# Kernel tuning notes

Hardware: AMD Instinct MI355X
Metric: run time of the kernel (lower is better)

Reference implementation:

```python
import jax, jax.numpy as jnp
import numpy as np

B, NI, NO = 4, 256, 256          # batch, num_in, num_out
DIN, DQ, DH, DOUT = 256, 256, 256, 256


def setup_inputs() -> dict:
    key = jax.random.key(0)
    ks = jax.random.split(key, 6)
    def w(k, shape, fan_in):
        return jax.random.normal(k, shape, jnp.float32) / np.sqrt(fan_in).astype(np.float32)
    return {
        "x": jax.random.normal(ks[0], (B, NI, DIN), jnp.float32),
        "query": jax.random.normal(ks[1], (B, NO, DQ), jnp.float32),
        # pre_cond_mlp: Linear(DIN -> DH)
        "W_pre": w(ks[2], (DIN, DH), DIN), "b_pre": jnp.zeros((DH,), jnp.float32),
        # cond_embed: Linear(DQ -> DH)
        "W_emb": w(ks[3], (DQ, DH), DQ), "b_emb": jnp.zeros((DH,), jnp.float32),
        # post_cond_mlp: Linear(2*DH -> DH) + GELU + Linear(DH -> DOUT)
        "W1": w(ks[4], (2 * DH, DH), 2 * DH), "b1": jnp.zeros((DH,), jnp.float32),
        "W2": w(ks[5], (DH, DOUT), DH), "b2": jnp.zeros((DOUT,), jnp.float32),
    }


def reference(x, query, W_pre, b_pre, W_emb, b_emb, W1, b1, W2, b2):
    # pre_cond_mlp(x): [B, NI, DH]
    xp = x @ W_pre + b_pre
    # cond_embed(query): [B, NO, DH]
    c = query @ W_emb + b_emb
    # Original torch code: repeat xp over NO, c over NI, concat -> [B,NI,NO,2*DH],
    # then Linear(2*DH->DH). Algebraically identical (and far cheaper) to split W1
    # and broadcast-add the two projections:
    W1x, W1c = W1[:DH], W1[DH:]          # [DH, DH] each
    h = (xp @ W1x)[:, :, None, :] + (c @ W1c)[:, None, :, :] + b1  # [B, NI, NO, DH]
    h = jax.nn.gelu(h, approximate=False)  # torch nn.GELU default = exact erf
    return h @ W2 + b2                     # [B, NI, NO, DOUT]
```

## Files before the change

kernel.cpp:

```cpp
#include <hip/hip_runtime.h>
#include <hip/hip_bf16.h>
#include <cstdint>
#include <cstddef>


typedef __bf16  bf16x8 __attribute__((ext_vector_type(8)));
typedef float   f32x16 __attribute__((ext_vector_type(16)));

__device__ __forceinline__ float fast_gelu(float x) {
    const float x2 = x * x;
    const float t  = __builtin_fmaf(x2, 0.07135481283f, 1.5957691216f);
    const float e  = __builtin_amdgcn_exp2f(x * t * -1.442695041f);
    return x * __builtin_amdgcn_rcpf(1.0f + e);
}

__global__ __launch_bounds__(256) void prep_kernel(
    const float* __restrict__ x, const float* __restrict__ query,
    const float* __restrict__ W_pre, const float* __restrict__ b_pre,
    const float* __restrict__ W_emb, const float* __restrict__ b_emb,
    const float* __restrict__ W1, const float* __restrict__ b1,
    const float* __restrict__ W2,
    float* __restrict__ u, float* __restrict__ v,
    unsigned short* __restrict__ w2t)
{
    const int b = blockIdx.x;
    const int t = threadIdx.x;

    if (b >= 512) {
        const int n0 = (b - 512) * 4;
        const float4 wv = *reinterpret_cast<const float4*>(W2 + (size_t)t * 256 + n0);
        const float vals[4] = {wv.x, wv.y, wv.z, wv.w};
#pragma unroll
        for (int j = 0; j < 4; ++j) {
            const __bf16 bv = (__bf16)vals[j];
            w2t[(size_t)(n0 + j) * 256 + t] = __builtin_bit_cast(unsigned short, bv);
        }
        return;
    }

    const bool isq = (b >= 256);
    const float* __restrict__ A   = isq ? query : x;
    const float* __restrict__ Wa  = isq ? W_emb : W_pre;
    const float* __restrict__ ba  = isq ? b_emb : b_pre;
    const float* __restrict__ W1p = isq ? (W1 + 256 * 256) : W1;
    float* __restrict__ outp      = isq ? v : u;
    const int r0 = (isq ? (b - 256) : b) * 4;

    __shared__ float as[4][256];
    __shared__ float xs[4][256];

#pragma unroll
    for (int r = 0; r < 4; ++r)
        as[r][t] = A[(size_t)(r0 + r) * 256 + t];
    __syncthreads();

    float acc[4] = {0.f, 0.f, 0.f, 0.f};
    for (int k = 0; k < 256; ++k) {
        const float wv = Wa[(size_t)k * 256 + t];
#pragma unroll
        for (int r = 0; r < 4; ++r) acc[r] += as[r][k] * wv;
    }
    const float bav = ba[t];
#pragma unroll
    for (int r = 0; r < 4; ++r) xs[r][t] = acc[r] + bav;
    __syncthreads();

    float acc2[4] = {0.f, 0.f, 0.f, 0.f};
    for (int k = 0; k < 256; ++k) {
        const float wv = W1p[(size_t)k * 256 + t];
#pragma unroll
        for (int r = 0; r < 4; ++r) acc2[r] += xs[r][k] * wv;
    }
    const float b1v = isq ? 0.f : b1[t];
#pragma unroll
    for (int r = 0; r < 4; ++r)
        outp[(size_t)(r0 + r) * 256 + t] = acc2[r] + b1v;
}

__global__ __launch_bounds__(256, 2) void fused_kernel(
    const float* __restrict__ U, const float* __restrict__ V,
    const unsigned short* __restrict__ W2T, const float* __restrict__ b2,
    float* __restrict__ out)
{
    __shared__ uint4 wlds[2048];

    const int t    = threadIdx.x;
    const int lane = t & 63;
    const int w    = t >> 6;
    const int l31  = lane & 31;
    const int hi   = lane >> 5;

    const size_t r0 = (size_t)blockIdx.x * 128;
    const int bb = (int)(r0 >> 16);
    const int ii = (int)((r0 >> 8) & 255);
    const int j0 = (int)(r0 & 255);

    const float* __restrict__ urow = U + ((size_t)(bb * 256 + ii)) * 256;
    const int jA = j0 + w * 32 + l31;
    const float* __restrict__ vrow = V + ((size_t)(bb * 256 + jA)) * 256;

    f32x16 acc[8];
#pragma unroll
    for (int i = 0; i < 8; ++i) acc[i] = (f32x16)0.f;

    for (int kk = 0; kk < 256; kk += 64) {
        __syncthreads();
#pragma unroll
        for (int it = 0; it < 8; ++it) {
            const int idx = it * 256 + t;
            const int n   = idx >> 3;
            const int g   = idx & 7;
            wlds[n * 8 + (g ^ (n & 7))] = *reinterpret_cast<const uint4*>(
                W2T + (size_t)n * 256 + kk + g * 8);
        }
        __syncthreads();

#pragma unroll
        for (int s = 0; s < 4; ++s) {
            const int k0 = kk + s * 16;
            const float4 u0 = *reinterpret_cast<const float4*>(urow + k0 + hi * 8);
            const float4 u1 = *reinterpret_cast<const float4*>(urow + k0 + hi * 8 + 4);
            const float4 v0 = *reinterpret_cast<const float4*>(vrow + k0 + hi * 8);
            const float4 v1 = *reinterpret_cast<const float4*>(vrow + k0 + hi * 8 + 4);
            const float hv[8] = {u0.x + v0.x, u0.y + v0.y, u0.z + v0.z, u0.w + v0.w,
                                 u1.x + v1.x, u1.y + v1.y, u1.z + v1.z, u1.w + v1.w};
            bf16x8 afrag;
#pragma unroll
            for (int e = 0; e < 8; ++e)
                afrag[e] = (__bf16)fast_gelu(hv[e]);

            const int gk = s * 2 + hi;
#pragma unroll
            for (int cg = 0; cg < 8; ++cg) {
                const int col = cg * 32 + l31;
                const bf16x8 bfrag = __builtin_bit_cast(
                    bf16x8, wlds[col * 8 + (gk ^ (col & 7))]);
                acc[cg] = __builtin_amdgcn_mfma_f32_32x32x16_bf16(
                    afrag, bfrag, acc[cg], 0, 0, 0);
            }
        }
    }

#pragma unroll
    for (int cg = 0; cg < 8; ++cg) {
        const int col = cg * 32 + l31;
        const float bv = b2[col];
#pragma unroll
        for (int r = 0; r < 16; ++r) {
            const int row = w * 32 + 4 * hi + (r & 3) + 8 * (r >> 2);
            out[(r0 + row) * 256 + col] = acc[cg][r] + bv;
        }
    }
}

extern "C" void kernel_launch(void* const* d_in, const int* in_sizes, int n_in,
                              void* d_out, int out_size, void* d_ws, size_t ws_size,
                              hipStream_t stream)
{
    const float* x     = (const float*)d_in[0];
    const float* query = (const float*)d_in[1];
    const float* W_pre = (const float*)d_in[2];
    const float* b_pre = (const float*)d_in[3];
    const float* W_emb = (const float*)d_in[4];
    const float* b_emb = (const float*)d_in[5];
    const float* W1    = (const float*)d_in[6];
    const float* b1    = (const float*)d_in[7];
    const float* W2    = (const float*)d_in[8];
    const float* b2    = (const float*)d_in[9];
    float* out = (float*)d_out;

    char* ws = (char*)d_ws;
    float* u            = (float*)(ws);
    float* v            = (float*)(ws + (1 << 20));
    unsigned short* w2t = (unsigned short*)(ws + 2 * (1 << 20));

    prep_kernel<<<576, 256, 0, stream>>>(x, query, W_pre, b_pre, W_emb, b_emb,
                                         W1, b1, W2, u, v, w2t);
    fused_kernel<<<2048, 256, 0, stream>>>(u, v, w2t, b2, out);
}
```

Before: 112.7 us.

## Halve fused tile rows, stage GELU activations in LDS, raise occupancy

The fused kernel now processes 64 output rows per block instead of 128. The four waves are arranged as a 2x2 grid over row and column halves, so each wave keeps 4 accumulators instead of 8. The GELU activations are computed once per element and staged in a swizzled LDS buffer, rather than recomputed per wave from global U/V. Launch bounds rise to 4 blocks per CU, GELU constants are folded to save a multiply, and output stores become nontemporal. The smaller tiles mean twice as many blocks and twice the total W2T loads into LDS.

```diff
diff --git a/kernel.cpp b/kernel.cpp
--- a/kernel.cpp
+++ b/kernel.cpp
@@ -9,8 +9,8 @@
 
 __device__ __forceinline__ float fast_gelu(float x) {
     const float x2 = x * x;
-    const float t  = __builtin_fmaf(x2, 0.07135481283f, 1.5957691216f);
-    const float e  = __builtin_amdgcn_exp2f(x * t * -1.442695041f);
+    const float m  = __builtin_fmaf(x2, -0.1029433f, -2.3022072f);
+    const float e  = __builtin_amdgcn_exp2f(x * m);
     return x * __builtin_amdgcn_rcpf(1.0f + e);
 }
 
@@ -77,34 +77,39 @@
         outp[(size_t)(r0 + r) * 256 + t] = acc2[r] + b1v;
 }
 
-__global__ __launch_bounds__(256, 2) void fused_kernel(
+__global__ __launch_bounds__(256, 4) void fused_kernel(
     const float* __restrict__ U, const float* __restrict__ V,
     const unsigned short* __restrict__ W2T, const float* __restrict__ b2,
     float* __restrict__ out)
 {
     __shared__ uint4 wlds[2048];
+    __shared__ uint4 hlds[512];
 
     const int t    = threadIdx.x;
     const int lane = t & 63;
     const int w    = t >> 6;
     const int l31  = lane & 31;
     const int hi   = lane >> 5;
+    const int rg   = w >> 1;
+    const int cgrp = w & 1;
 
-    const size_t r0 = (size_t)blockIdx.x * 128;
+    const size_t r0 = (size_t)blockIdx.x * 64;
     const int bb = (int)(r0 >> 16);
     const int ii = (int)((r0 >> 8) & 255);
     const int j0 = (int)(r0 & 255);
 
+    const int hr = t >> 2;
+    const int kq = t & 3;
     const float* __restrict__ urow = U + ((size_t)(bb * 256 + ii)) * 256;
-    const int jA = j0 + w * 32 + l31;
-    const float* __restrict__ vrow = V + ((size_t)(bb * 256 + jA)) * 256;
+    const float* __restrict__ vrow = V + ((size_t)(bb * 256 + j0 + hr)) * 256;
 
-    f32x16 acc[8];
+    const int arow = rg * 32 + l31;
+
+    f32x16 acc[4];
 #pragma unroll
-    for (int i = 0; i < 8; ++i) acc[i] = (f32x16)0.f;
+    for (int i = 0; i < 4; ++i) acc[i] = (f32x16)0.f;
 
     for (int kk = 0; kk < 256; kk += 64) {
-        __syncthreads();
 #pragma unroll
         for (int it = 0; it < 8; ++it) {
             const int idx = it * 256 + t;
@@ -113,42 +118,55 @@
             wlds[n * 8 + (g ^ (n & 7))] = *reinterpret_cast<const uint4*>(
                 W2T + (size_t)n * 256 + kk + g * 8);
         }
+        bf16x8 h0, h1;
+#pragma unroll
+        for (int m = 0; m < 4; ++m) {
+            const float4 uv = *reinterpret_cast<const float4*>(urow + kk + kq * 16 + m * 4);
+            const float4 vv = *reinterpret_cast<const float4*>(vrow + kk + kq * 16 + m * 4);
+            const float g0 = fast_gelu(uv.x + vv.x);
+            const float g1 = fast_gelu(uv.y + vv.y);
+            const float g2 = fast_gelu(uv.z + vv.z);
+            const float g3 = fast_gelu(uv.w + vv.w);
+            if (m < 2) {
+                const int e = m * 4;
+                h0[e] = (__bf16)g0; h0[e+1] = (__bf16)g1;
+                h0[e+2] = (__bf16)g2; h0[e+3] = (__bf16)g3;
+            } else {
+                const int e = (m - 2) * 4;
+                h1[e] = (__bf16)g0; h1[e+1] = (__bf16)g1;
+                h1[e+2] = (__bf16)g2; h1[e+3] = (__bf16)g3;
+            }
+        }
+        hlds[hr * 8 + ((kq * 2)     ^ (hr & 7))] = __builtin_bit_cast(uint4, h0);
+        hlds[hr * 8 + ((kq * 2 + 1) ^ (hr & 7))] = __builtin_bit_cast(uint4, h1);
         __syncthreads();
 
 #pragma unroll
         for (int s = 0; s < 4; ++s) {
-            const int k0 = kk + s * 16;
-            const float4 u0 = *reinterpret_cast<const float4*>(urow + k0 + hi * 8);
-            const float4 u1 = *reinterpret_cast<const float4*>(urow + k0 + hi * 8 + 4);
-            const float4 v0 = *reinterpret_cast<const float4*>(vrow + k0 + hi * 8);
-            const float4 v1 = *reinterpret_cast<const float4*>(vrow + k0 + hi * 8 + 4);
-            const float hv[8] = {u0.x + v0.x, u0.y + v0.y, u0.z + v0.z, u0.w + v0.w,
-                                 u1.x + v1.x, u1.y + v1.y, u1.z + v1.z, u1.w + v1.w};
-            bf16x8 afrag;
+            const int g = 2 * s + hi;
+            const bf16x8 afrag = __builtin_bit_cast(
+                bf16x8, hlds[arow * 8 + (g ^ (arow & 7))]);
 #pragma unroll
-            for (int e = 0; e < 8; ++e)
-                afrag[e] = (__bf16)fast_gelu(hv[e]);
-
-            const int gk = s * 2 + hi;
-#pragma unroll
-            for (int cg = 0; cg < 8; ++cg) {
-                const int col = cg * 32 + l31;
+            for (int cg = 0; cg < 4; ++cg) {
+                const int col = cgrp * 128 + cg * 32 + l31;
                 const bf16x8 bfrag = __builtin_bit_cast(
-                    bf16x8, wlds[col * 8 + (gk ^ (col & 7))]);
+                    bf16x8, wlds[col * 8 + (g ^ (col & 7))]);
                 acc[cg] = __builtin_amdgcn_mfma_f32_32x32x16_bf16(
                     afrag, bfrag, acc[cg], 0, 0, 0);
             }
         }
+        __syncthreads();
     }
 
 #pragma unroll
-    for (int cg = 0; cg < 8; ++cg) {
-        const int col = cg * 32 + l31;
+    for (int cg = 0; cg < 4; ++cg) {
+        const int col = cgrp * 128 + cg * 32 + l31;
         const float bv = b2[col];
 #pragma unroll
-        for (int r = 0; r < 16; ++r) {
-            const int row = w * 32 + 4 * hi + (r & 3) + 8 * (r >> 2);
-            out[(r0 + row) * 256 + col] = acc[cg][r] + bv;
+        for (int rr = 0; rr < 16; ++rr) {
+            const int row = rg * 32 + 4 * hi + (rr & 3) + 8 * (rr >> 2);
+            __builtin_nontemporal_store(acc[cg][rr] + bv,
+                                        out + (r0 + row) * 256 + col);
         }
     }
 }
@@ -176,5 +194,5 @@
 
     prep_kernel<<<576, 256, 0, stream>>>(x, query, W_pre, b_pre, W_emb, b_emb,
                                          W1, b1, W2, u, v, w2t);
-    fused_kernel<<<2048, 256, 0, stream>>>(u, v, w2t, b2, out);
+    fused_kernel<<<4096, 256, 0, stream>>>(u, v, w2t, b2, out);
 }
```

Measured after the change: 126.4 us. +12.2%, slower.

## Stage GELU activations through LDS with coalesced loads and async W2 copies

Applied to the files above, without the earlier changes.

V rows are now loaded coalesced (float2 across the 32 lanes along k) instead of each lane streaming its own row. GELU is computed once per element and packed to bf16 into a swizzled LDS tile that the MFMA A-fragments read from. W2T tiles are copied with global_load_lds direct-to-LDS transfers, the GELU constants are folded to save a multiply, and output stores become nontemporal. This adds 16KB of LDS per block, which may reduce occupancy, and moves the barriers to the end of each k-step.

```diff
diff --git a/kernel.cpp b/kernel.cpp
--- a/kernel.cpp
+++ b/kernel.cpp
@@ -9,8 +9,8 @@
 
 __device__ __forceinline__ float fast_gelu(float x) {
     const float x2 = x * x;
-    const float t  = __builtin_fmaf(x2, 0.07135481283f, 1.5957691216f);
-    const float e  = __builtin_amdgcn_exp2f(x * t * -1.442695041f);
+    const float m  = __builtin_fmaf(x2, -0.1029433f, -2.3022072f);
+    const float e  = __builtin_amdgcn_exp2f(x * m);
     return x * __builtin_amdgcn_rcpf(1.0f + e);
 }
 
@@ -83,6 +83,8 @@
     float* __restrict__ out)
 {
     __shared__ uint4 wlds[2048];
+    __shared__ uint4 hlds[1024];
+    unsigned int* const hlds32 = reinterpret_cast<unsigned int*>(hlds);
 
     const int t    = threadIdx.x;
     const int lane = t & 63;
@@ -95,41 +97,52 @@
     const int ii = (int)((r0 >> 8) & 255);
     const int j0 = (int)(r0 & 255);
 
-    const float* __restrict__ urow = U + ((size_t)(bb * 256 + ii)) * 256;
-    const int jA = j0 + w * 32 + l31;
-    const float* __restrict__ vrow = V + ((size_t)(bb * 256 + jA)) * 256;
+    const float* __restrict__ urow  = U + ((size_t)(bb * 256 + ii)) * 256;
+    const float* __restrict__ vbase = V + ((size_t)(bb * 256 + j0)) * 256;
 
     f32x16 acc[8];
 #pragma unroll
     for (int i = 0; i < 8; ++i) acc[i] = (f32x16)0.f;
 
     for (int kk = 0; kk < 256; kk += 64) {
-        __syncthreads();
 #pragma unroll
         for (int it = 0; it < 8; ++it) {
             const int idx = it * 256 + t;
             const int n   = idx >> 3;
-            const int g   = idx & 7;
-            wlds[n * 8 + (g ^ (n & 7))] = *reinterpret_cast<const uint4*>(
-                W2T + (size_t)n * 256 + kk + g * 8);
+            const int gp  = idx & 7;
+            const int g   = gp ^ (n & 7);
+            __builtin_amdgcn_global_load_lds(
+                (const __attribute__((address_space(1))) unsigned int*)
+                    (W2T + (size_t)n * 256 + kk + g * 8),
+                (__attribute__((address_space(3))) unsigned int*)
+                    (wlds + idx),
+                16, 0, 0);
+        }
+
+        const float2 uv2 = *reinterpret_cast<const float2*>(urow + kk + 2 * l31);
+        float2 vv[16];
+#pragma unroll
+        for (int p = 0; p < 16; ++p) {
+            const int row = w * 32 + p * 2 + hi;
+            vv[p] = *reinterpret_cast<const float2*>(vbase + (size_t)row * 256 + kk + 2 * l31);
+        }
+#pragma unroll
+        for (int p = 0; p < 16; ++p) {
+            const int row = w * 32 + p * 2 + hi;
+            union { unsigned int u32; __bf16 h[2]; } pk;
+            pk.h[0] = (__bf16)fast_gelu(uv2.x + vv[p].x);
+            pk.h[1] = (__bf16)fast_gelu(uv2.y + vv[p].y);
+            const int d = l31;
+            hlds32[row * 32 + (((d >> 2) ^ (row & 7)) << 2) + (d & 3)] = pk.u32;
         }
         __syncthreads();
 
 #pragma unroll
         for (int s = 0; s < 4; ++s) {
-            const int k0 = kk + s * 16;
-            const float4 u0 = *reinterpret_cast<const float4*>(urow + k0 + hi * 8);
-            const float4 u1 = *reinterpret_cast<const float4*>(urow + k0 + hi * 8 + 4);
-            const float4 v0 = *reinterpret_cast<const float4*>(vrow + k0 + hi * 8);
-            const float4 v1 = *reinterpret_cast<const float4*>(vrow + k0 + hi * 8 + 4);
-            const float hv[8] = {u0.x + v0.x, u0.y + v0.y, u0.z + v0.z, u0.w + v0.w,
-                                 u1.x + v1.x, u1.y + v1.y, u1.z + v1.z, u1.w + v1.w};
-            bf16x8 afrag;
-#pragma unroll
-            for (int e = 0; e < 8; ++e)
-                afrag[e] = (__bf16)fast_gelu(hv[e]);
-
-            const int gk = s * 2 + hi;
+            const int gk = 2 * s + hi;
+            const int arow = w * 32 + l31;
+            const bf16x8 afrag = __builtin_bit_cast(
+                bf16x8, hlds[arow * 8 + (gk ^ (arow & 7))]);
 #pragma unroll
             for (int cg = 0; cg < 8; ++cg) {
                 const int col = cg * 32 + l31;
@@ -139,6 +152,7 @@
                     afrag, bfrag, acc[cg], 0, 0, 0);
             }
         }
+        __syncthreads();
     }
 
 #pragma unroll
@@ -146,9 +160,10 @@
         const int col = cg * 32 + l31;
         const float bv = b2[col];
 #pragma unroll
-        for (int r = 0; r < 16; ++r) {
-            const int row = w * 32 + 4 * hi + (r & 3) + 8 * (r >> 2);
-            out[(r0 + row) * 256 + col] = acc[cg][r] + bv;
+        for (int rr = 0; rr < 16; ++rr) {
+            const int row = w * 32 + 4 * hi + (rr & 3) + 8 * (rr >> 2);
+            __builtin_nontemporal_store(acc[cg][rr] + bv,
+                                        out + (r0 + row) * 256 + col);
         }
     }
 }
```

Result: faster. 106.5 us (-5.5%).

## Split output columns across blocks and stage full-K W2 tile in LDS asynchronously

Applied to the files above, without the earlier changes.

Each block of the fused kernel now covers 128 rows by 128 output columns instead of 128 by 256, which doubles the grid. The block loads its whole 256-deep slice of W2 into LDS once with global_load_lds, replacing four sync-separated staging rounds with a single barrier. Output stores are marked nontemporal, and the GELU exponent constants are pre-folded to save a multiply. The trade-off is that the GELU of each U+V element is now computed in two blocks, and LDS use doubles, which may lower occupancy.

```diff
diff --git a/kernel.cpp b/kernel.cpp
--- a/kernel.cpp
+++ b/kernel.cpp
@@ -9,8 +9,8 @@
 
 __device__ __forceinline__ float fast_gelu(float x) {
     const float x2 = x * x;
-    const float t  = __builtin_fmaf(x2, 0.07135481283f, 1.5957691216f);
-    const float e  = __builtin_amdgcn_exp2f(x * t * -1.442695041f);
+    const float m  = __builtin_fmaf(x2, -0.1029433f, -2.3022072f);
+    const float e  = __builtin_amdgcn_exp2f(x * m);
     return x * __builtin_amdgcn_rcpf(1.0f + e);
 }
 
@@ -82,7 +82,7 @@
     const unsigned short* __restrict__ W2T, const float* __restrict__ b2,
     float* __restrict__ out)
 {
-    __shared__ uint4 wlds[2048];
+    __shared__ uint4 wlds[4096];
 
     const int t    = threadIdx.x;
     const int lane = t & 63;
@@ -90,65 +90,77 @@
     const int l31  = lane & 31;
     const int hi   = lane >> 5;
 
-    const size_t r0 = (size_t)blockIdx.x * 128;
-    const int bb = (int)(r0 >> 16);
-    const int ii = (int)((r0 >> 8) & 255);
-    const int j0 = (int)(r0 & 255);
-
-    const float* __restrict__ urow = U + ((size_t)(bb * 256 + ii)) * 256;
-    const int jA = j0 + w * 32 + l31;
-    const float* __restrict__ vrow = V + ((size_t)(bb * 256 + jA)) * 256;
-
-    f32x16 acc[8];
-#pragma unroll
-    for (int i = 0; i < 8; ++i) acc[i] = (f32x16)0.f;
-
-    for (int kk = 0; kk < 256; kk += 64) {
-        __syncthreads();
-#pragma unroll
-        for (int it = 0; it < 8; ++it) {
-            const int idx = it * 256 + t;
-            const int n   = idx >> 3;
-            const int g   = idx & 7;
-            wlds[n * 8 + (g ^ (n & 7))] = *reinterpret_cast<const uint4*>(
-                W2T + (size_t)n * 256 + kk + g * 8);
-        }
-        __syncthreads();
+    const int bid  = blockIdx.x;
+    const int tile = bid >> 2;
+    const int jh   = (bid >> 1) & 1;
+    const int ch   = bid & 1;
+    const int bb   = tile >> 8;
+    const int n0   = ch * 128;
+    const int j0   = jh * 128;
 
 #pragma unroll
-        for (int s = 0; s < 4; ++s) {
-            const int k0 = kk + s * 16;
-            const float4 u0 = *reinterpret_cast<const float4*>(urow + k0 + hi * 8);
-            const float4 u1 = *reinterpret_cast<const float4*>(urow + k0 + hi * 8 + 4);
-            const float4 v0 = *reinterpret_cast<const float4*>(vrow + k0 + hi * 8);
-            const float4 v1 = *reinterpret_cast<const float4*>(vrow + k0 + hi * 8 + 4);
-            const float hv[8] = {u0.x + v0.x, u0.y + v0.y, u0.z + v0.z, u0.w + v0.w,
-                                 u1.x + v1.x, u1.y + v1.y, u1.z + v1.z, u1.w + v1.w};
-            bf16x8 afrag;
+    for (int it = 0; it < 16; ++it) {
+        const int idx = it * 256 + t;
+        const int n   = idx >> 5;
+        const int gp  = idx & 31;
+        const int g   = (gp & 24) | ((gp ^ n) & 7);
+        __builtin_amdgcn_global_load_lds(
+            (const __attribute__((address_space(1))) unsigned int*)
+                (W2T + (size_t)(n0 + n) * 256 + g * 8),
+            (__attribute__((address_space(3))) unsigned int*)(wlds + idx),
+            16, 0, 0);
+    }
+
+    const float* __restrict__ urow = U + (size_t)tile * 256;
+    const float* __restrict__ vrow =
+        V + ((size_t)(bb * 256 + j0 + w * 32 + l31)) * 256;
+
+    f32x16 acc[4];
 #pragma unroll
-            for (int e = 0; e < 8; ++e)
-                afrag[e] = (__bf16)fast_gelu(hv[e]);
+    for (int i = 0; i < 4; ++i) acc[i] = (f32x16)0.f;
 
-            const int gk = s * 2 + hi;
+    __syncthreads();
+
+#pragma unroll 4
+    for (int s = 0; s < 16; ++s) {
+        const int k0 = s * 16 + hi * 8;
+        const float4 ua = *reinterpret_cast<const float4*>(urow + k0);
+        const float4 ub = *reinterpret_cast<const float4*>(urow + k0 + 4);
+        const float4 va = *reinterpret_cast<const float4*>(vrow + k0);
+        const float4 vb = *reinterpret_cast<const float4*>(vrow + k0 + 4);
+
+        bf16x8 afrag;
+        afrag[0] = (__bf16)fast_gelu(ua.x + va.x);
+        afrag[1] = (__bf16)fast_gelu(ua.y + va.y);
+        afrag[2] = (__bf16)fast_gelu(ua.z + va.z);
+        afrag[3] = (__bf16)fast_gelu(ua.w + va.w);
+        afrag[4] = (__bf16)fast_gelu(ub.x + vb.x);
+        afrag[5] = (__bf16)fast_gelu(ub.y + vb.y);
+        afrag[6] = (__bf16)fast_gelu(ub.z + vb.z);
+        afrag[7] = (__bf16)fast_gelu(ub.w + vb.w);
+
+        const int gk = 2 * s + hi;
 #pragma unroll
-            for (int cg = 0; cg < 8; ++cg) {
-                const int col = cg * 32 + l31;
-                const bf16x8 bfrag = __builtin_bit_cast(
-                    bf16x8, wlds[col * 8 + (gk ^ (col & 7))]);
-                acc[cg] = __builtin_amdgcn_mfma_f32_32x32x16_bf16(
-                    afrag, bfrag, acc[cg], 0, 0, 0);
-            }
+        for (int cg = 0; cg < 4; ++cg) {
+            const int nloc = cg * 32 + l31;
+            const int slot = (gk & 24) | ((gk ^ nloc) & 7);
+            const bf16x8 bfrag = __builtin_bit_cast(
+                bf16x8, wlds[nloc * 32 + slot]);
+            acc[cg] = __builtin_amdgcn_mfma_f32_32x32x16_bf16(
+                afrag, bfrag, acc[cg], 0, 0, 0);
         }
     }
 
+    const size_t obase = (size_t)tile << 16;
 #pragma unroll
-    for (int cg = 0; cg < 8; ++cg) {
-        const int col = cg * 32 + l31;
+    for (int cg = 0; cg < 4; ++cg) {
+        const int col = n0 + cg * 32 + l31;
         const float bv = b2[col];
 #pragma unroll
-        for (int r = 0; r < 16; ++r) {
-            const int row = w * 32 + 4 * hi + (r & 3) + 8 * (r >> 2);
-            out[(r0 + row) * 256 + col] = acc[cg][r] + bv;
+        for (int rr = 0; rr < 16; ++rr) {
+            const int row = j0 + w * 32 + 4 * hi + (rr & 3) + 8 * (rr >> 2);
+            __builtin_nontemporal_store(acc[cg][rr] + bv,
+                                        out + obase + (size_t)row * 256 + col);
         }
     }
 }
@@ -176,5 +188,5 @@
 
     prep_kernel<<<576, 256, 0, stream>>>(x, query, W_pre, b_pre, W_emb, b_emb,
                                          W1, b1, W2, u, v, w2t);
-    fused_kernel<<<2048, 256, 0, stream>>>(u, v, w2t, b2, out);
+    fused_kernel<<<4096, 256, 0, stream>>>(u, v, w2t, b2, out);
 }
```

Measured after the change: 129.6 us. 15.0% more time.
